# Performance work log

Measured on AMD Instinct MI355X. Metric: run time of the kernel, lower is better.

Reference implementation:

```python
import jax, jax.numpy as jnp
import numpy as np

N, E, B = 250000, 1000000, 500
FD = 78  # num_features_xd


def setup_inputs() -> dict:
    key = jax.random.key(0)
    ks = jax.random.split(key, 24)
    g = lambda i, shape, fan_in: jax.random.normal(ks[i], shape, jnp.float32) / np.sqrt(fan_in)
    inp = {
        "x": jax.random.normal(ks[0], (N, FD), jnp.float32),
        "edge_index": jax.random.randint(ks[1], (2, E), 0, N, jnp.int32),
        "batch": jnp.repeat(jnp.arange(B, dtype=jnp.int32), N // B),  # sorted, every graph non-empty
        "target": jax.random.randint(ks[2], (B, 1000), 0, 26, jnp.int32),
        # GCN layers
        "W1": g(3, (FD, FD), FD), "b1": jnp.zeros((FD,), jnp.float32),
        "W2": g(4, (FD, 2 * FD), FD), "b2": jnp.zeros((2 * FD,), jnp.float32),
        "W3": g(5, (2 * FD, 4 * FD), 2 * FD), "b3": jnp.zeros((4 * FD,), jnp.float32),
        # graph head
        "fcg1_w": g(6, (4 * FD, 1024), 4 * FD), "fcg1_b": jnp.zeros((1024,), jnp.float32),
        "fcg2_w": g(7, (1024, 128), 1024), "fcg2_b": jnp.zeros((128,), jnp.float32),
        # protein branch
        "emb": g(8, (26, 128), 1),
        "conv_w": g(9, (32, 1000, 8), 1000 * 8), "conv_b": jnp.zeros((32,), jnp.float32),
        "fcxt_w": g(10, (32 * 121, 128), 32 * 121), "fcxt_b": jnp.zeros((128,), jnp.float32),
        # fusion head
        "fc1_w": g(11, (256, 1024), 256), "fc1_b": jnp.zeros((1024,), jnp.float32),
        "fc2_w": g(12, (1024, 512), 1024), "fc2_b": jnp.zeros((512,), jnp.float32),
        "out_w": g(13, (512, 1), 512), "out_b": jnp.zeros((1,), jnp.float32),
    }
    return inp


def _gcn_conv(x, W, b, src, dst, dinv, n):
    # PyG GCNConv: out = D^-1/2 (A+I) D^-1/2 (x W) + b, symmetric norm with self-loops
    xw = x @ W
    norm = dinv[src] * dinv[dst]                                   # [E]
    agg = jax.ops.segment_sum(xw[src] * norm[:, None], dst, num_segments=n)
    agg = agg + xw * (dinv * dinv)[:, None]                        # self-loop term
    return agg + b


def reference(x, edge_index, batch, target,
              W1, b1, W2, b2, W3, b3,
              fcg1_w, fcg1_b, fcg2_w, fcg2_b,
              emb, conv_w, conv_b, fcxt_w, fcxt_b,
              fc1_w, fc1_b, fc2_w, fc2_b, out_w, out_b):
    n = x.shape[0]
    src, dst = edge_index[0], edge_index[1]
    # degree with self-loops (edge weights 1)
    deg = jax.ops.segment_sum(jnp.ones((src.shape[0],), x.dtype), dst, num_segments=n) + 1.0
    dinv = jax.lax.rsqrt(deg)

    h = jax.nn.relu(_gcn_conv(x, W1, b1, src, dst, dinv, n))
    h = jax.nn.relu(_gcn_conv(h, W2, b2, src, dst, dinv, n))
    h = jax.nn.relu(_gcn_conv(h, W3, b3, src, dst, dinv, n))

    bsz = fcg2_w.shape[1] * 0 + target.shape[0]  # B
    g = jax.ops.segment_max(h, batch, num_segments=bsz)            # global max pool -> [B, 312]
    g = jax.nn.relu(g @ fcg1_w + fcg1_b)
    g = g @ fcg2_w + fcg2_b                                        # dropout = identity (eval)

    # protein branch: Conv1d over embedding dim (channels = seq positions = 1000)
    e = emb[target]                                                # [B, 1000, 128]
    c = jax.lax.conv_general_dilated(e, conv_w, window_strides=(1,), padding="VALID",
                                     dimension_numbers=("NCH", "OIH", "NCH"))
    c = c + conv_b[None, :, None]                                  # [B, 32, 121]
    xt = c.reshape(bsz, 32 * 121) @ fcxt_w + fcxt_b

    xc = jnp.concatenate([g, xt], axis=1)                          # [B, 256]
    xc = jax.nn.relu(xc @ fc1_w + fc1_b)
    xc = jax.nn.relu(xc @ fc2_w + fc2_b)
    return xc @ out_w + out_b                                      # [B, 1]
```

## Files before the change

kernel.cpp:

```cpp
#include <hip/hip_runtime.h>
#include <hip/hip_bf16.h>

#define DEV_INLINE __device__ __forceinline__

static constexpr int Nn = 250000;
static constexpr int Ee = 1000000;
static constexpr int Bb = 500;
static constexpr int NPB = Nn / Bb;

typedef __attribute__((ext_vector_type(8))) short short8;
typedef __attribute__((ext_vector_type(4))) float f32x4;

DEV_INLINE float b2f(__hip_bfloat16 v) { return __bfloat162float(v); }
DEV_INLINE __hip_bfloat16 f2b(float v) { return __float2bfloat16(v); }
DEV_INLINE unsigned short f2bu(float v) {
    __hip_bfloat16 h = __float2bfloat16(v);
    return __builtin_bit_cast(unsigned short, h);
}
DEV_INLINE float bfu2f(unsigned short u) { return __uint_as_float(((unsigned)u) << 16); }

DEV_INLINE float2 ld2v(const float* p, size_t i) { return *(const float2*)(p + i); }
DEV_INLINE float2 ld2v(const __hip_bfloat16* p, size_t i) {
    ushort2 u = *(const ushort2*)(p + i);
    return make_float2(bfu2f(u.x), bfu2f(u.y));
}
DEV_INLINE float4 ld4v(const float* p, size_t i) { return *(const float4*)(p + i); }
DEV_INLINE float4 ld4v(const __hip_bfloat16* p, size_t i) {
    ushort4 u = *(const ushort4*)(p + i);
    return make_float4(bfu2f(u.x), bfu2f(u.y), bfu2f(u.z), bfu2f(u.w));
}
template <int G, typename TIN>
DEV_INLINE float4 ldg_vec(const TIN* p, size_t i) {
    if constexpr (G == 4) return ld4v(p, i);
    else { float2 v = ld2v(p, i); return make_float4(v.x, v.y, 0.f, 0.f); }
}

__global__ void k_deg(const int* __restrict__ dst, int* __restrict__ deg) {
    int i = blockIdx.x * 256 + threadIdx.x;
    if (i < Ee) atomicAdd(&deg[dst[i]], 1);
}

__global__ void k_dinv(const int* __restrict__ deg, float* __restrict__ dinv) {
    int i = blockIdx.x * 256 + threadIdx.x;
    if (i < Nn) dinv[i] = rsqrtf((float)deg[i] + 1.0f);
}

__global__ __launch_bounds__(256) void k_scan1(const int* __restrict__ deg,
                                               int* __restrict__ rp,
                                               int* __restrict__ bsum) {
    __shared__ int s[256];
    int t = threadIdx.x;
    int i = blockIdx.x * 256 + t;
    int v = (i < Nn) ? deg[i] : 0;
    s[t] = v;
    __syncthreads();
    for (int off = 1; off < 256; off <<= 1) {
        int x = (t >= off) ? s[t - off] : 0;
        __syncthreads();
        s[t] += x;
        __syncthreads();
    }
    if (i < Nn) rp[i] = s[t] - v;
    if (t == 255) bsum[blockIdx.x] = s[255];
}

__global__ __launch_bounds__(1024) void k_scan2(int* __restrict__ bsum, int nb) {
    __shared__ int s[1024];
    int t = threadIdx.x;
    int v = (t < nb) ? bsum[t] : 0;
    s[t] = v;
    __syncthreads();
    for (int off = 1; off < 1024; off <<= 1) {
        int x = (t >= off) ? s[t - off] : 0;
        __syncthreads();
        s[t] += x;
        __syncthreads();
    }
    if (t < nb) bsum[t] = s[t] - v;
}

__global__ void k_scan3(int* __restrict__ rp, int* __restrict__ cursor,
                        const int* __restrict__ bsum) {
    int i = blockIdx.x * 256 + threadIdx.x;
    if (i < Nn) {
        int v = rp[i] + bsum[blockIdx.x];
        rp[i] = v;
        cursor[i] = v;
    }
    if (i == 0) rp[Nn] = Ee;
}

__global__ void k_scatter(const int* __restrict__ src, const int* __restrict__ dst,
                          const float* __restrict__ dinv, int* __restrict__ cursor,
                          int* __restrict__ col, float* __restrict__ enorm) {
    int i = blockIdx.x * 256 + threadIdx.x;
    if (i >= Ee) return;
    int s = src[i], d = dst[i];
    int pos = atomicAdd(&cursor[d], 1);
    col[pos] = s;
    enorm[pos] = dinv[s] * dinv[d];
}

template <int K, int F, int KP, int FP>
__global__ __launch_bounds__(64) void k_wprep(const float* __restrict__ W,
                                              unsigned short* __restrict__ Wb) {
    constexpr int KSTEPS = KP / 32;
    const int nt = blockIdx.x, ks = blockIdx.y;
    const int l = threadIdx.x;
    const int n = nt * 16 + (l & 15);
    unsigned short* o = Wb + ((size_t)(nt * KSTEPS + ks) * 64 + l) * 8;
#pragma unroll
    for (int j = 0; j < 8; ++j) {
        const int k = (l >> 4) * 8 + j + ks * 32;
        o[j] = (k < K && n < F) ? f2bu(W[(size_t)k * F + n]) : (unsigned short)0;
    }
}

template <int K, int KP, int F, int FP, bool POOL, typename TIN>
__global__ __launch_bounds__(320) void k_gcn(const TIN* __restrict__ in,
                                             const int* __restrict__ rp,
                                             const int* __restrict__ col,
                                             const float* __restrict__ enorm,
                                             const float* __restrict__ dinv,
                                             const unsigned short* __restrict__ Wb,
                                             const float* __restrict__ bias,
                                             __hip_bfloat16* __restrict__ out,
                                             float* __restrict__ gpool) {
    constexpr int ROWS = 16, BD = 320, WAVES = 5;
    constexpr int G = (K % 4 == 0) ? 4 : 2;
    constexpr int CPR = K / G;
    constexpr int SLOTS = CPR * ROWS;
    constexpr int ECAP = 16 * ROWS;
    constexpr int KSTEPS = KP / 32;
    constexpr int NT = FP / 16;
    constexpr int TPW = NT / WAVES;
    static_assert(FP % (16 * WAVES) == 0 && KP % 32 == 0 && K % G == 0, "pad");

    __shared__ alignas(16) unsigned short sh[ROWS * KP];
    __shared__ int sRp[ROWS + 1];
    __shared__ int sCol[ECAP];
    __shared__ float sEn[ECAP];

    const int i0 = blockIdx.x * ROWS;
    const int t = threadIdx.x;

    if (t <= ROWS) sRp[t] = rp[i0 + t];
    const int base = rp[i0];
    const int ne = rp[i0 + ROWS] - base;
    if (ne <= ECAP) {
        for (int e = t; e < ne; e += BD) {
            sCol[e] = col[base + e];
            sEn[e] = enorm[base + e];
        }
    }
    for (int e = t; e < ROWS * (KP - K); e += BD) {
        const int r = e / (KP - K);
        sh[r * KP + K + (e - r * (KP - K))] = 0;
    }
    __syncthreads();

    for (int slot = t; slot < SLOTS; slot += BD) {
        const int r = slot / CPR;
        const int c = slot - r * CPR;
        const int i = i0 + r;
        const size_t coff = (size_t)G * c;
        const float di = dinv[i];
        const float selfw = di * di;
        float4 acc = ldg_vec<G>(in, (size_t)i * K + coff);
        acc.x *= selfw; acc.y *= selfw; acc.z *= selfw; acc.w *= selfw;

        const int e0a = sRp[r], e1a = sRp[r + 1];
        if (ne <= ECAP) {
            int j = e0a - base;
            const int jend = e1a - base;
            for (; j + 4 <= jend; j += 4) {
                const int n0 = sCol[j + 0], n1 = sCol[j + 1], n2 = sCol[j + 2], n3 = sCol[j + 3];
                const float w0 = sEn[j + 0], w1 = sEn[j + 1], w2 = sEn[j + 2], w3 = sEn[j + 3];
                float4 v0 = ldg_vec<G>(in, (size_t)n0 * K + coff);
                float4 v1 = ldg_vec<G>(in, (size_t)n1 * K + coff);
                float4 v2 = ldg_vec<G>(in, (size_t)n2 * K + coff);
                float4 v3 = ldg_vec<G>(in, (size_t)n3 * K + coff);
                acc.x += v0.x * w0 + v1.x * w1 + v2.x * w2 + v3.x * w3;
                acc.y += v0.y * w0 + v1.y * w1 + v2.y * w2 + v3.y * w3;
                acc.z += v0.z * w0 + v1.z * w1 + v2.z * w2 + v3.z * w3;
                acc.w += v0.w * w0 + v1.w * w1 + v2.w * w2 + v3.w * w3;
            }
            for (; j < jend; ++j) {
                const int n = sCol[j];
                const float w = sEn[j];
                float4 v = ldg_vec<G>(in, (size_t)n * K + coff);
                acc.x += v.x * w; acc.y += v.y * w; acc.z += v.z * w; acc.w += v.w * w;
            }
        } else {
            for (int j = e0a; j < e1a; ++j) {
                const int n = col[j];
                const float w = enorm[j];
                float4 v = ldg_vec<G>(in, (size_t)n * K + coff);
                acc.x += v.x * w; acc.y += v.y * w; acc.z += v.z * w; acc.w += v.w * w;
            }
        }
        if constexpr (G == 4) {
            ushort4 u;
            u.x = f2bu(acc.x); u.y = f2bu(acc.y); u.z = f2bu(acc.z); u.w = f2bu(acc.w);
            *(ushort4*)&sh[r * KP + 4 * c] = u;
        } else {
            ushort2 u;
            u.x = f2bu(acc.x); u.y = f2bu(acc.y);
            *(ushort2*)&sh[r * KP + 2 * c] = u;
        }
    }
    __syncthreads();

    const int w = t >> 6, lane = t & 63;
    const int arow = lane & 15, aquad = lane >> 4;
    short8 afr[KSTEPS];
#pragma unroll
    for (int ks = 0; ks < KSTEPS; ++ks)
        afr[ks] = *(const short8*)&sh[arow * KP + aquad * 8 + ks * 32];

#pragma unroll
    for (int nti = 0; nti < TPW; ++nti) {
        const int nt = w * TPW + nti;
        const short8* bp = (const short8*)Wb + (size_t)nt * KSTEPS * 64 + lane;
        f32x4 acc = {0.f, 0.f, 0.f, 0.f};
#pragma unroll
        for (int ks = 0; ks < KSTEPS; ++ks) {
            short8 bfr = bp[ks * 64];
            acc = __builtin_amdgcn_mfma_f32_16x16x32_bf16(afr[ks], bfr, acc, 0, 0, 0);
        }
        const int f = nt * 16 + arow;
        if (f < F) {
            const float bv = bias[f];
            float v0 = fmaxf(acc[0] + bv, 0.f);
            float v1 = fmaxf(acc[1] + bv, 0.f);
            float v2 = fmaxf(acc[2] + bv, 0.f);
            float v3 = fmaxf(acc[3] + bv, 0.f);
            const int ib = i0 + aquad * 4;
            if constexpr (!POOL) {
                out[(size_t)(ib + 0) * F + f] = f2b(v0);
                out[(size_t)(ib + 1) * F + f] = f2b(v1);
                out[(size_t)(ib + 2) * F + f] = f2b(v2);
                out[(size_t)(ib + 3) * F + f] = f2b(v3);
            } else {
                const int g0 = ib / NPB, g3 = (ib + 3) / NPB;
                if (g0 == g3) {
                    float m = fmaxf(fmaxf(v0, v1), fmaxf(v2, v3));
                    atomicMax((int*)&gpool[g0 * F + f], __float_as_int(m));
                } else {
                    float av[4] = {v0, v1, v2, v3};
#pragma unroll
                    for (int r = 0; r < 4; ++r)
                        atomicMax((int*)&gpool[((ib + r) / NPB) * F + f], __float_as_int(av[r]));
                }
            }
        }
    }
}

template <int K, int FOUT, int KS, bool RELU, int BD>
__global__ __launch_bounds__(BD) void k_fc(const float* __restrict__ in,
                                           const float* __restrict__ W,
                                           const float* __restrict__ bias,
                                           float* __restrict__ out,
                                           int ostride, int ooff) {
    static_assert(!(RELU && KS > 1), "cannot split K with fused ReLU");
    static_assert(K % KS == 0, "K must divide evenly");
    constexpr int KC = K / KS;
    const int j = blockIdx.x * BD + threadIdx.x;
    const int b = blockIdx.y;
    const int z = blockIdx.z;
    const float* __restrict__ inp = in + (size_t)b * K + z * KC;
    const float* __restrict__ Wp = W + (size_t)(z * KC) * FOUT + j;
    float acc = (z == 0) ? bias[j] : 0.f;
#pragma unroll 8
    for (int k = 0; k < KC; ++k) acc += inp[k] * Wp[(size_t)k * FOUT];
    float* dst = &out[(size_t)b * ostride + ooff + j];
    if (KS > 1) {
        atomicAdd(dst, acc);
    } else {
        *dst = RELU ? fmaxf(acc, 0.f) : acc;
    }
}

__global__ __launch_bounds__(128) void k_P(const float* __restrict__ emb,
                                           const float* __restrict__ fcxt_w,
                                           float* __restrict__ P) {
    const int v = blockIdx.x, o = blockIdx.y;
    const int j = threadIdx.x;
    __shared__ float se[128];
    se[j] = emb[v * 128 + j];
    __syncthreads();
    float acc[8];
#pragma unroll
    for (int k = 0; k < 8; ++k) acc[k] = 0.f;
    const float* fw = fcxt_w + (size_t)(o * 121) * 128 + j;
#pragma unroll 4
    for (int h = 0; h < 121; ++h) {
        const float f = fw[(size_t)h * 128];
#pragma unroll
        for (int k = 0; k < 8; ++k) acc[k] += se[h + k] * f;
    }
    float* Pp = P + ((size_t)(v * 32 + o) * 8) * 128 + j;
#pragma unroll
    for (int k = 0; k < 8; ++k) Pp[(size_t)k * 128] = acc[k];
}

__global__ __launch_bounds__(128) void k_T(const float* __restrict__ convw,
                                           const float* __restrict__ P,
                                           float* __restrict__ T) {
    const int i0 = blockIdx.x * 8;
    const int v = blockIdx.y;
    const int t = threadIdx.x;
    __shared__ float wt[8 * 256];
    for (int e = t; e < 2048; e += 128) {
        const int r = e >> 8;
        const int kk = e & 255;
        wt[e] = convw[(size_t)(kk >> 3) * 8000 + (size_t)(i0 + r) * 8 + (kk & 7)];
    }
    __syncthreads();
    float acc[8];
#pragma unroll
    for (int r = 0; r < 8; ++r) acc[r] = 0.f;
    const float* Pp = P + (size_t)v * 256 * 128 + t;
#pragma unroll 2
    for (int kk = 0; kk < 256; ++kk) {
        const float pv = Pp[(size_t)kk * 128];
#pragma unroll
        for (int r = 0; r < 8; ++r) acc[r] += wt[r * 256 + kk] * pv;
    }
    float* Tp = T + ((size_t)v * 1000 + i0) * 128 + t;
#pragma unroll
    for (int r = 0; r < 8; ++r) Tp[(size_t)r * 128] = acc[r];
}

__global__ __launch_bounds__(128) void k_C0(const float* __restrict__ fcxt_w,
                                            const float* __restrict__ fcxt_b,
                                            const float* __restrict__ convb,
                                            float* __restrict__ C0) {
    const int o = blockIdx.x;
    const int j = threadIdx.x;
    float acc = 0.f;
    const float* fw = fcxt_w + (size_t)(o * 121) * 128 + j;
#pragma unroll 4
    for (int h = 0; h < 121; ++h) acc += fw[(size_t)h * 128];
    acc *= convb[o];
    if (o == 0) acc += fcxt_b[j];
    atomicAdd(&C0[j], acc);
}

template <int ZS>
__global__ __launch_bounds__(128) void k_xt(const int* __restrict__ target,
                                            const float* __restrict__ T,
                                            const float* __restrict__ C0,
                                            float* __restrict__ xc) {
    constexpr int CH = 1000 / ZS;
    const int b = blockIdx.x;
    const int z = blockIdx.y;
    const int j = threadIdx.x;
    const int* tg = target + b * 1000 + z * CH;
    float acc = (z == 0) ? C0[j] : 0.f;
    int i = 0;
    for (; i + 4 <= CH; i += 4) {
        const int v0 = tg[i + 0], v1 = tg[i + 1], v2 = tg[i + 2], v3 = tg[i + 3];
        const int ib = z * CH + i;
        acc += T[((size_t)v0 * 1000 + ib + 0) * 128 + j]
             + T[((size_t)v1 * 1000 + ib + 1) * 128 + j]
             + T[((size_t)v2 * 1000 + ib + 2) * 128 + j]
             + T[((size_t)v3 * 1000 + ib + 3) * 128 + j];
    }
    for (; i < CH; ++i) {
        acc += T[((size_t)tg[i] * 1000 + z * CH + i) * 128 + j];
    }
    atomicAdd(&xc[(size_t)b * 256 + 128 + j], acc);
}

__global__ __launch_bounds__(64) void k_out(const float* __restrict__ in,
                                            const float* __restrict__ w,
                                            const float* __restrict__ ob,
                                            float* __restrict__ out) {
    const int b = blockIdx.x;
    const int lane = threadIdx.x;
    const float* p = in + (size_t)b * 512;
    float acc = 0.f;
#pragma unroll
    for (int i = 0; i < 8; ++i) acc += p[lane + 64 * i] * w[lane + 64 * i];
    for (int off = 32; off > 0; off >>= 1) acc += __shfl_down(acc, off);
    if (lane == 0) out[b] = acc + ob[0];
}

extern "C" void kernel_launch(void* const* d_in, const int* in_sizes, int n_in,
                              void* d_out, int out_size, void* d_ws, size_t ws_size,
                              hipStream_t stream) {
    (void)in_sizes; (void)n_in; (void)out_size; (void)ws_size;
    const float* x      = (const float*)d_in[0];
    const int* ei       = (const int*)d_in[1];
    const int* target   = (const int*)d_in[3];
    const float* W1     = (const float*)d_in[4];
    const float* b1     = (const float*)d_in[5];
    const float* W2     = (const float*)d_in[6];
    const float* b2     = (const float*)d_in[7];
    const float* W3     = (const float*)d_in[8];
    const float* b3     = (const float*)d_in[9];
    const float* fcg1_w = (const float*)d_in[10];
    const float* fcg1_b = (const float*)d_in[11];
    const float* fcg2_w = (const float*)d_in[12];
    const float* fcg2_b = (const float*)d_in[13];
    const float* emb    = (const float*)d_in[14];
    const float* conv_w = (const float*)d_in[15];
    const float* conv_b = (const float*)d_in[16];
    const float* fcxt_w = (const float*)d_in[17];
    const float* fcxt_b = (const float*)d_in[18];
    const float* fc1_w  = (const float*)d_in[19];
    const float* fc1_b  = (const float*)d_in[20];
    const float* fc2_w  = (const float*)d_in[21];
    const float* fc2_b  = (const float*)d_in[22];
    const float* out_w  = (const float*)d_in[23];
    const float* out_b  = (const float*)d_in[24];

    const int* src = ei;
    const int* dst = ei + Ee;

    size_t off = 0;
    auto alloc = [&](size_t bytes) -> void* {
        off = (off + 255) & ~(size_t)255;
        void* p = (char*)d_ws + off;
        off += bytes;
        return p;
    };
    int*   deg    = (int*)alloc((size_t)Nn * 4);
    float* dinv   = (float*)alloc((size_t)Nn * 4);
    int*   rp     = (int*)alloc((size_t)(Nn + 1) * 4);
    int*   col    = (int*)alloc((size_t)Ee * 4);
    float* enorm  = (float*)alloc((size_t)Ee * 4);
    int*   bsum   = (int*)alloc(1024 * 4);
    unsigned short* Wb1 = (unsigned short*)alloc((size_t)5 * 3 * 64 * 8 * 2);
    unsigned short* Wb2 = (unsigned short*)alloc((size_t)10 * 3 * 64 * 8 * 2);
    unsigned short* Wb3 = (unsigned short*)alloc((size_t)20 * 5 * 64 * 8 * 2);
    __hip_bfloat16* h1 = (__hip_bfloat16*)alloc((size_t)Nn * 78 * 2);
    __hip_bfloat16* h2 = (__hip_bfloat16*)alloc((size_t)Nn * 156 * 2);
    int* cursor = deg;

    size_t hoff = 0;
    auto halloc = [&](size_t bytes) -> void* {
        hoff = (hoff + 255) & ~(size_t)255;
        void* p = (char*)h1 + hoff;
        hoff += bytes;
        return p;
    };
    float* gpool = (float*)halloc((size_t)Bb * 312 * 4);
    float* g1    = (float*)halloc((size_t)Bb * 1024 * 4);
    float* xc    = (float*)halloc((size_t)Bb * 256 * 4);
    float* f1    = (float*)halloc((size_t)Bb * 1024 * 4);
    float* f2    = (float*)halloc((size_t)Bb * 512 * 4);
    float* C0    = (float*)halloc(128 * 4);
    float* Pbuf  = (float*)halloc((size_t)26 * 32 * 8 * 128 * 4);
    float* Tbuf  = (float*)halloc((size_t)26 * 1000 * 128 * 4);

    const int nb = (Nn + 255) / 256;

    hipMemsetAsync(deg, 0, (size_t)Nn * 4, stream);
    k_deg<<<(Ee + 255) / 256, 256, 0, stream>>>(dst, deg);
    k_dinv<<<nb, 256, 0, stream>>>(deg, dinv);
    k_scan1<<<nb, 256, 0, stream>>>(deg, rp, bsum);
    k_scan2<<<1, 1024, 0, stream>>>(bsum, nb);
    k_scan3<<<nb, 256, 0, stream>>>(rp, cursor, bsum);
    k_scatter<<<(Ee + 255) / 256, 256, 0, stream>>>(src, dst, dinv, cursor, col, enorm);

    k_wprep<78, 78, 96, 80><<<dim3(5, 3), 64, 0, stream>>>(W1, Wb1);
    k_wprep<78, 156, 96, 160><<<dim3(10, 3), 64, 0, stream>>>(W2, Wb2);
    k_wprep<156, 312, 160, 320><<<dim3(20, 5), 64, 0, stream>>>(W3, Wb3);

    k_gcn<78, 96, 78, 80, false><<<Nn / 16, 320, 0, stream>>>(x, rp, col, enorm, dinv, Wb1, b1, h1, (float*)nullptr);
    k_gcn<78, 96, 156, 160, false><<<Nn / 16, 320, 0, stream>>>(h1, rp, col, enorm, dinv, Wb2, b2, h2, (float*)nullptr);
    hipMemsetAsync(gpool, 0, (size_t)Bb * 312 * 4, stream);
    k_gcn<156, 160, 312, 320, true><<<Nn / 16, 320, 0, stream>>>(h2, rp, col, enorm, dinv, Wb3, b3, (__hip_bfloat16*)nullptr, gpool);

    hipMemsetAsync(C0, 0, 128 * 4, stream);
    hipMemsetAsync(xc, 0, (size_t)Bb * 256 * 4, stream);
    k_P<<<dim3(26, 32), 128, 0, stream>>>(emb, fcxt_w, Pbuf);
    k_T<<<dim3(125, 26), 128, 0, stream>>>(conv_w, Pbuf, Tbuf);
    k_C0<<<32, 128, 0, stream>>>(fcxt_w, fcxt_b, conv_b, C0);
    k_xt<8><<<dim3(Bb, 8), 128, 0, stream>>>(target, Tbuf, C0, xc);

    k_fc<312, 1024, 1, true, 256><<<dim3(4, Bb, 1), 256, 0, stream>>>(gpool, fcg1_w, fcg1_b, g1, 1024, 0);
    k_fc<1024, 128, 2, false, 128><<<dim3(1, Bb, 2), 128, 0, stream>>>(g1, fcg2_w, fcg2_b, xc, 256, 0);

    k_fc<256, 1024, 1, true, 256><<<dim3(4, Bb, 1), 256, 0, stream>>>(xc, fc1_w, fc1_b, f1, 1024, 0);
    k_fc<1024, 512, 1, true, 256><<<dim3(2, Bb, 1), 256, 0, stream>>>(f1, fc2_w, fc2_b, f2, 512, 0);
    k_out<<<Bb, 64, 0, stream>>>(f2, out_w, out_b, (float*)d_out);
}
```

Before: 991.5 us.

## Pad activations to 8-element bf16 rows, convert x to bf16, reduce pooling atomics

Adds a kernel that converts the fp32 node features to bf16 with rows padded to 80. Hidden activations are stored with padded strides of 80 and 160 so every gather becomes a 16-byte load of 8 bf16 values instead of float4/float2 pieces. Layer 1 now reads bf16 x instead of fp32, roughly halving its gather traffic. The pooling epilogue combines the max across lanes with shuffles when a 16-row tile lies in one graph, cutting atomics. The cost is an extra conversion pass, slightly more memory for the padding, and x rounded to bf16 before layer 1.

```diff
diff --git a/kernel.cpp b/kernel.cpp
--- a/kernel.cpp
+++ b/kernel.cpp
@@ -9,6 +9,7 @@
 static constexpr int NPB = Nn / Bb;
 
 typedef __attribute__((ext_vector_type(8))) short short8;
+typedef __attribute__((ext_vector_type(8))) unsigned short ushort8v;
 typedef __attribute__((ext_vector_type(4))) float f32x4;
 
 DEV_INLINE float b2f(__hip_bfloat16 v) { return __bfloat162float(v); }
@@ -18,22 +19,6 @@
     return __builtin_bit_cast(unsigned short, h);
 }
 DEV_INLINE float bfu2f(unsigned short u) { return __uint_as_float(((unsigned)u) << 16); }
-
-DEV_INLINE float2 ld2v(const float* p, size_t i) { return *(const float2*)(p + i); }
-DEV_INLINE float2 ld2v(const __hip_bfloat16* p, size_t i) {
-    ushort2 u = *(const ushort2*)(p + i);
-    return make_float2(bfu2f(u.x), bfu2f(u.y));
-}
-DEV_INLINE float4 ld4v(const float* p, size_t i) { return *(const float4*)(p + i); }
-DEV_INLINE float4 ld4v(const __hip_bfloat16* p, size_t i) {
-    ushort4 u = *(const ushort4*)(p + i);
-    return make_float4(bfu2f(u.x), bfu2f(u.y), bfu2f(u.z), bfu2f(u.w));
-}
-template <int G, typename TIN>
-DEV_INLINE float4 ldg_vec(const TIN* p, size_t i) {
-    if constexpr (G == 4) return ld4v(p, i);
-    else { float2 v = ld2v(p, i); return make_float4(v.x, v.y, 0.f, 0.f); }
-}
 
 __global__ void k_deg(const int* __restrict__ dst, int* __restrict__ deg) {
     int i = blockIdx.x * 256 + threadIdx.x;
@@ -101,6 +86,21 @@
     enorm[pos] = dinv[s] * dinv[d];
 }
 
+__global__ void k_xprep(const float* __restrict__ x, unsigned short* __restrict__ xb) {
+    int gid = blockIdx.x * 256 + threadIdx.x;
+    if (gid >= Nn * 20) return;
+    int i = gid / 20;
+    int c = gid - 20 * i;
+    int k = 4 * c;
+    const float* xp = x + (size_t)i * 78;
+    ushort4 u;
+    u.x = (k + 0 < 78) ? f2bu(xp[k + 0]) : (unsigned short)0;
+    u.y = (k + 1 < 78) ? f2bu(xp[k + 1]) : (unsigned short)0;
+    u.z = (k + 2 < 78) ? f2bu(xp[k + 2]) : (unsigned short)0;
+    u.w = (k + 3 < 78) ? f2bu(xp[k + 3]) : (unsigned short)0;
+    *(ushort4*)&xb[(size_t)i * 80 + k] = u;
+}
+
 template <int K, int F, int KP, int FP>
 __global__ __launch_bounds__(64) void k_wprep(const float* __restrict__ W,
                                               unsigned short* __restrict__ Wb) {
@@ -116,8 +116,8 @@
     }
 }
 
-template <int K, int KP, int F, int FP, bool POOL, typename TIN>
-__global__ __launch_bounds__(320) void k_gcn(const TIN* __restrict__ in,
+template <int KIN, int KP, int F, int FP, int SOUT, bool POOL>
+__global__ __launch_bounds__(320) void k_gcn(const __hip_bfloat16* __restrict__ in_,
                                              const int* __restrict__ rp,
                                              const int* __restrict__ col,
                                              const float* __restrict__ enorm,
@@ -127,14 +127,14 @@
                                              __hip_bfloat16* __restrict__ out,
                                              float* __restrict__ gpool) {
     constexpr int ROWS = 16, BD = 320, WAVES = 5;
-    constexpr int G = (K % 4 == 0) ? 4 : 2;
-    constexpr int CPR = K / G;
+    constexpr int CPR = KIN / 8;
     constexpr int SLOTS = CPR * ROWS;
     constexpr int ECAP = 16 * ROWS;
     constexpr int KSTEPS = KP / 32;
     constexpr int NT = FP / 16;
     constexpr int TPW = NT / WAVES;
-    static_assert(FP % (16 * WAVES) == 0 && KP % 32 == 0 && K % G == 0, "pad");
+    static_assert(KIN % 8 == 0 && KP % 32 == 0 && KP >= KIN && FP % (16 * WAVES) == 0, "pad");
+    const unsigned short* in = (const unsigned short*)in_;
 
     __shared__ alignas(16) unsigned short sh[ROWS * KP];
     __shared__ int sRp[ROWS + 1];
@@ -153,9 +153,11 @@
             sEn[e] = enorm[base + e];
         }
     }
-    for (int e = t; e < ROWS * (KP - K); e += BD) {
-        const int r = e / (KP - K);
-        sh[r * KP + K + (e - r * (KP - K))] = 0;
+    if constexpr (KP > KIN) {
+        for (int e = t; e < ROWS * (KP - KIN); e += BD) {
+            const int r = e / (KP - KIN);
+            sh[r * KP + KIN + (e - r * (KP - KIN))] = 0;
+        }
     }
     __syncthreads();
 
@@ -163,12 +165,15 @@
         const int r = slot / CPR;
         const int c = slot - r * CPR;
         const int i = i0 + r;
-        const size_t coff = (size_t)G * c;
+        const size_t coff = (size_t)8 * c;
         const float di = dinv[i];
         const float selfw = di * di;
-        float4 acc = ldg_vec<G>(in, (size_t)i * K + coff);
-        acc.x *= selfw; acc.y *= selfw; acc.z *= selfw; acc.w *= selfw;
-
+        float acc[8];
+        {
+            ushort8v s = *(const ushort8v*)(in + (size_t)i * KIN + coff);
+#pragma unroll
+            for (int j = 0; j < 8; ++j) acc[j] = bfu2f(s[j]) * selfw;
+        }
         const int e0a = sRp[r], e1a = sRp[r + 1];
         if (ne <= ECAP) {
             int j = e0a - base;
@@ -176,38 +181,35 @@
             for (; j + 4 <= jend; j += 4) {
                 const int n0 = sCol[j + 0], n1 = sCol[j + 1], n2 = sCol[j + 2], n3 = sCol[j + 3];
                 const float w0 = sEn[j + 0], w1 = sEn[j + 1], w2 = sEn[j + 2], w3 = sEn[j + 3];
-                float4 v0 = ldg_vec<G>(in, (size_t)n0 * K + coff);
-                float4 v1 = ldg_vec<G>(in, (size_t)n1 * K + coff);
-                float4 v2 = ldg_vec<G>(in, (size_t)n2 * K + coff);
-                float4 v3 = ldg_vec<G>(in, (size_t)n3 * K + coff);
-                acc.x += v0.x * w0 + v1.x * w1 + v2.x * w2 + v3.x * w3;
-                acc.y += v0.y * w0 + v1.y * w1 + v2.y * w2 + v3.y * w3;
-                acc.z += v0.z * w0 + v1.z * w1 + v2.z * w2 + v3.z * w3;
-                acc.w += v0.w * w0 + v1.w * w1 + v2.w * w2 + v3.w * w3;
+                ushort8v a0 = *(const ushort8v*)(in + (size_t)n0 * KIN + coff);
+                ushort8v a1 = *(const ushort8v*)(in + (size_t)n1 * KIN + coff);
+                ushort8v a2 = *(const ushort8v*)(in + (size_t)n2 * KIN + coff);
+                ushort8v a3 = *(const ushort8v*)(in + (size_t)n3 * KIN + coff);
+#pragma unroll
+                for (int q = 0; q < 8; ++q)
+                    acc[q] += bfu2f(a0[q]) * w0 + bfu2f(a1[q]) * w1 +
+                              bfu2f(a2[q]) * w2 + bfu2f(a3[q]) * w3;
             }
             for (; j < jend; ++j) {
                 const int n = sCol[j];
                 const float w = sEn[j];
-                float4 v = ldg_vec<G>(in, (size_t)n * K + coff);
-                acc.x += v.x * w; acc.y += v.y * w; acc.z += v.z * w; acc.w += v.w * w;
+                ushort8v a = *(const ushort8v*)(in + (size_t)n * KIN + coff);
+#pragma unroll
+                for (int q = 0; q < 8; ++q) acc[q] += bfu2f(a[q]) * w;
             }
         } else {
             for (int j = e0a; j < e1a; ++j) {
                 const int n = col[j];
                 const float w = enorm[j];
-                float4 v = ldg_vec<G>(in, (size_t)n * K + coff);
-                acc.x += v.x * w; acc.y += v.y * w; acc.z += v.z * w; acc.w += v.w * w;
+                ushort8v a = *(const ushort8v*)(in + (size_t)n * KIN + coff);
+#pragma unroll
+                for (int q = 0; q < 8; ++q) acc[q] += bfu2f(a[q]) * w;
             }
         }
-        if constexpr (G == 4) {
-            ushort4 u;
-            u.x = f2bu(acc.x); u.y = f2bu(acc.y); u.z = f2bu(acc.z); u.w = f2bu(acc.w);
-            *(ushort4*)&sh[r * KP + 4 * c] = u;
-        } else {
-            ushort2 u;
-            u.x = f2bu(acc.x); u.y = f2bu(acc.y);
-            *(ushort2*)&sh[r * KP + 2 * c] = u;
-        }
+        ushort8v o;
+#pragma unroll
+        for (int q = 0; q < 8; ++q) o[q] = f2bu(acc[q]);
+        *(ushort8v*)&sh[r * KP + 8 * c] = o;
     }
     __syncthreads();
 
@@ -217,6 +219,8 @@
 #pragma unroll
     for (int ks = 0; ks < KSTEPS; ++ks)
         afr[ks] = *(const short8*)&sh[arow * KP + aquad * 8 + ks * 32];
+
+    const bool uni = (i0 / NPB) == ((i0 + ROWS - 1) / NPB);
 
 #pragma unroll
     for (int nti = 0; nti < TPW; ++nti) {
@@ -229,28 +233,39 @@
             acc = __builtin_amdgcn_mfma_f32_16x16x32_bf16(afr[ks], bfr, acc, 0, 0, 0);
         }
         const int f = nt * 16 + arow;
-        if (f < F) {
-            const float bv = bias[f];
-            float v0 = fmaxf(acc[0] + bv, 0.f);
-            float v1 = fmaxf(acc[1] + bv, 0.f);
-            float v2 = fmaxf(acc[2] + bv, 0.f);
-            float v3 = fmaxf(acc[3] + bv, 0.f);
-            const int ib = i0 + aquad * 4;
-            if constexpr (!POOL) {
-                out[(size_t)(ib + 0) * F + f] = f2b(v0);
-                out[(size_t)(ib + 1) * F + f] = f2b(v1);
-                out[(size_t)(ib + 2) * F + f] = f2b(v2);
-                out[(size_t)(ib + 3) * F + f] = f2b(v3);
-            } else {
+        const int ib = i0 + aquad * 4;
+        if constexpr (!POOL) {
+            if (f < F) {
+                const float bv = bias[f];
+#pragma unroll
+                for (int r = 0; r < 4; ++r)
+                    out[(size_t)(ib + r) * SOUT + f] = f2b(fmaxf(acc[r] + bv, 0.f));
+            } else if (f < SOUT) {
+#pragma unroll
+                for (int r = 0; r < 4; ++r)
+                    out[(size_t)(ib + r) * SOUT + f] = f2b(0.f);
+            }
+        } else {
+            float m = 0.f, v[4];
+            const float bv = (f < F) ? bias[f] : 0.f;
+#pragma unroll
+            for (int r = 0; r < 4; ++r) {
+                v[r] = fmaxf(acc[r] + bv, 0.f);
+                m = fmaxf(m, v[r]);
+            }
+            if (uni) {
+                m = fmaxf(m, __shfl_xor(m, 16));
+                m = fmaxf(m, __shfl_xor(m, 32));
+                if (aquad == 0 && f < F)
+                    atomicMax((int*)&gpool[(i0 / NPB) * F + f], __float_as_int(m));
+            } else if (f < F) {
                 const int g0 = ib / NPB, g3 = (ib + 3) / NPB;
                 if (g0 == g3) {
-                    float m = fmaxf(fmaxf(v0, v1), fmaxf(v2, v3));
                     atomicMax((int*)&gpool[g0 * F + f], __float_as_int(m));
                 } else {
-                    float av[4] = {v0, v1, v2, v3};
 #pragma unroll
                     for (int r = 0; r < 4; ++r)
-                        atomicMax((int*)&gpool[((ib + r) / NPB) * F + f], __float_as_int(av[r]));
+                        atomicMax((int*)&gpool[((ib + r) / NPB) * F + f], __float_as_int(v[r]));
                 }
             }
         }
@@ -436,9 +451,10 @@
     unsigned short* Wb1 = (unsigned short*)alloc((size_t)5 * 3 * 64 * 8 * 2);
     unsigned short* Wb2 = (unsigned short*)alloc((size_t)10 * 3 * 64 * 8 * 2);
     unsigned short* Wb3 = (unsigned short*)alloc((size_t)20 * 5 * 64 * 8 * 2);
-    __hip_bfloat16* h1 = (__hip_bfloat16*)alloc((size_t)Nn * 78 * 2);
-    __hip_bfloat16* h2 = (__hip_bfloat16*)alloc((size_t)Nn * 156 * 2);
+    __hip_bfloat16* h1 = (__hip_bfloat16*)alloc((size_t)Nn * 80 * 2);
+    __hip_bfloat16* h2 = (__hip_bfloat16*)alloc((size_t)Nn * 160 * 2);
     int* cursor = deg;
+    unsigned short* xb = (unsigned short*)h2;
 
     size_t hoff = 0;
     auto halloc = [&](size_t bytes) -> void* {
@@ -458,6 +474,8 @@
 
     const int nb = (Nn + 255) / 256;
 
+    k_xprep<<<(Nn * 20 + 255) / 256, 256, 0, stream>>>(x, xb);
+
     hipMemsetAsync(deg, 0, (size_t)Nn * 4, stream);
     k_deg<<<(Ee + 255) / 256, 256, 0, stream>>>(dst, deg);
     k_dinv<<<nb, 256, 0, stream>>>(deg, dinv);
@@ -470,10 +488,13 @@
     k_wprep<78, 156, 96, 160><<<dim3(10, 3), 64, 0, stream>>>(W2, Wb2);
     k_wprep<156, 312, 160, 320><<<dim3(20, 5), 64, 0, stream>>>(W3, Wb3);
 
-    k_gcn<78, 96, 78, 80, false><<<Nn / 16, 320, 0, stream>>>(x, rp, col, enorm, dinv, Wb1, b1, h1, (float*)nullptr);
-    k_gcn<78, 96, 156, 160, false><<<Nn / 16, 320, 0, stream>>>(h1, rp, col, enorm, dinv, Wb2, b2, h2, (float*)nullptr);
+    k_gcn<80, 96, 78, 80, 80, false><<<Nn / 16, 320, 0, stream>>>(
+        (const __hip_bfloat16*)xb, rp, col, enorm, dinv, Wb1, b1, h1, (float*)nullptr);
+    k_gcn<80, 96, 156, 160, 160, false><<<Nn / 16, 320, 0, stream>>>(
+        h1, rp, col, enorm, dinv, Wb2, b2, h2, (float*)nullptr);
     hipMemsetAsync(gpool, 0, (size_t)Bb * 312 * 4, stream);
-    k_gcn<156, 160, 312, 320, true><<<Nn / 16, 320, 0, stream>>>(h2, rp, col, enorm, dinv, Wb3, b3, (__hip_bfloat16*)nullptr, gpool);
+    k_gcn<160, 160, 312, 320, 0, true><<<Nn / 16, 320, 0, stream>>>(
+        h2, rp, col, enorm, dinv, Wb3, b3, (__hip_bfloat16*)nullptr, gpool);
 
     hipMemsetAsync(C0, 0, 128 * 4, stream);
     hipMemsetAsync(xc, 0, (size_t)Bb * 256 * 4, stream);
```

New measurement: 886.3 us. 1.12x faster.
